# Kernel tuning notes

Hardware: AMD Instinct MI355X
Metric: run time of the kernel (lower is better)

The kernel has to match this reference:

```python
import jax, jax.numpy as jnp
import numpy as np

N = 16                      # input_dim (state dimension)
EPS = 1e-6
TRIL_R, TRIL_C = np.tril_indices(N)   # 136 lower-triangular slots


def setup_inputs() -> dict:
    key = jax.random.key(0)
    ks = jax.random.split(key, 7)
    B = 131072
    def xavier(k, fan_in, fan_out):
        lim = float(np.sqrt(6.0 / (fan_in + fan_out)))
        return jax.random.uniform(k, (fan_in, fan_out), jnp.float32, -lim, lim)
    return {
        "points": jax.random.normal(ks[0], (B, N), jnp.float32),
        "W0": xavier(ks[1], N, 512),
        "b0": jax.random.normal(ks[2], (512,), jnp.float32) * 0.01,
        "W1": xavier(ks[3], 512, 512),
        "b1": jax.random.normal(ks[4], (512,), jnp.float32) * 0.01,
        "W2": xavier(ks[5], 512, 136),
        "b2": jax.random.normal(ks[6], (136,), jnp.float32) * 0.01,
    }


def reference(points, W0, b0, W1, b1, W2, b2):
    # MLP: tanh, tanh, identity
    h = jnp.tanh(points @ W0 + b0)
    h = jnp.tanh(h @ W1 + b1)
    net = h @ W2 + b2                         # [B, 136] tril entries
    B = points.shape[0]
    # Batched scatter into lower-triangular matrices M: [B, N, N]
    M = jnp.zeros((B, N, N), points.dtype).at[:, TRIL_R, TRIL_C].set(net)
    # x^T (M M^T) x == ||M^T x||^2
    y = jnp.einsum('bij,bi->bj', M, points)   # (M^T x)_j = sum_i M_ij x_i
    vals = jnp.sum(y * y, axis=-1) + EPS * jnp.sum(points * points, axis=-1)
    return vals.reshape(-1, 1)
```

## Files before the change

kernel.cpp:

```cpp
#include <hip/hip_runtime.h>

typedef __bf16 bf16x4 __attribute__((ext_vector_type(4)));
typedef __bf16 bf16x8 __attribute__((ext_vector_type(8)));
typedef float f32x16 __attribute__((ext_vector_type(16)));

#define W0F_OFF 0
#define W1F_OFF 8192
#define W2F_OFF (8192 + 262144)
#define PREP_TOTAL (8192 + 262144 + 81920)

__global__ void prep_weights(const float* __restrict__ W0,
                             const float* __restrict__ W1,
                             const float* __restrict__ W2,
                             __bf16* __restrict__ ws) {
    int t = blockIdx.x * 256 + threadIdx.x;
    if (t < 8192) {
        int j = t & 7, lane = (t >> 3) & 63, nt = t >> 9;
        int n = nt * 32 + (lane & 31);
        int k = (lane >> 5) * 8 + j;
        ws[W0F_OFF + t] = (__bf16)W0[k * 512 + n];
    } else if (t < 8192 + 262144) {
        int u = t - 8192;
        int j = u & 7, lane = (u >> 3) & 63;
        int x = u >> 9;
        int kk = x & 31, nt = x >> 5;
        int n = nt * 32 + (lane & 31);
        int k = kk * 16 + (lane >> 5) * 8 + j;
        ws[W1F_OFF + u] = (__bf16)W1[k * 512 + n];
    } else if (t < PREP_TOTAL) {
        int v = t - (8192 + 262144);
        int j = v & 7, lane = (v >> 3) & 63;
        int x = v >> 9;
        int kk = x & 31, nt = x >> 5;
        int n = nt * 32 + (lane & 31);
        int k = kk * 16 + (lane >> 5) * 8 + j;
        ws[W2F_OFF + v] = (n < 136) ? (__bf16)W2[k * 136 + n] : (__bf16)0.0f;
    }
}

__device__ __forceinline__ float fast_tanh(float x) {
#if __has_builtin(__builtin_amdgcn_exp2f)
    float e = __builtin_amdgcn_exp2f(x * 2.885390081777926f);
#else
    float e = exp2f(x * 2.885390081777926f);
#endif
    return 1.0f - 2.0f * __builtin_amdgcn_rcpf(e + 1.0f);
}

#define HSTR 520
#define NSTR 140

__global__ __launch_bounds__(256, 2)
void fused_mlp_quad(const float* __restrict__ points,
                    const float* __restrict__ b0,
                    const float* __restrict__ b1,
                    const float* __restrict__ b2,
                    const __bf16* __restrict__ ws,
                    float* __restrict__ out) {
    __shared__ __align__(16) unsigned char lds_raw[33280];
    __bf16* h  = (__bf16*)lds_raw;
    float* net = (float*)lds_raw;

    const __bf16* w0f = ws + W0F_OFF;
    const __bf16* w1f = ws + W1F_OFF;
    const __bf16* w2f = ws + W2F_OFF;

    const int tid = threadIdx.x;
    const int w   = tid >> 6;
    const int l   = tid & 63;
    const int ln  = l & 31;
    const int hi  = l >> 5;
    const int row0 = blockIdx.x * 32;

    const int lofs = l * 8;

    {
        const float* src = points + (row0 + ln) * 16 + hi * 8;
        float4 p0 = ((const float4*)src)[0];
        float4 p1 = ((const float4*)src)[1];
        bf16x8 bx;
        bx[0] = (__bf16)p0.x; bx[1] = (__bf16)p0.y; bx[2] = (__bf16)p0.z; bx[3] = (__bf16)p0.w;
        bx[4] = (__bf16)p1.x; bx[5] = (__bf16)p1.y; bx[6] = (__bf16)p1.z; bx[7] = (__bf16)p1.w;
#pragma unroll
        for (int t = 0; t < 4; ++t) {
            const int ntg = w * 4 + t;
            bf16x8 wf = *(const bf16x8*)(w0f + ntg * 512 + lofs);
            f32x16 acc = {};
            acc = __builtin_amdgcn_mfma_f32_32x32x16_bf16(wf, bx, acc, 0, 0, 0);
#pragma unroll
            for (int rg = 0; rg < 4; ++rg) {
                const int n0 = ntg * 32 + 8 * rg + 4 * hi;
                float4 bias = *(const float4*)(b0 + n0);
                bf16x4 v;
                v[0] = (__bf16)fast_tanh(acc[4 * rg + 0] + bias.x);
                v[1] = (__bf16)fast_tanh(acc[4 * rg + 1] + bias.y);
                v[2] = (__bf16)fast_tanh(acc[4 * rg + 2] + bias.z);
                v[3] = (__bf16)fast_tanh(acc[4 * rg + 3] + bias.w);
                *(bf16x4*)(h + ln * HSTR + n0) = v;
            }
        }
    }
    __syncthreads();

    f32x16 acc1[4] = {};
    {
        const __bf16* arow = h + ln * HSTR + hi * 8;
        const __bf16* w1b0 = w1f + (w * 4 + 0) * 16384 + lofs;
        const __bf16* w1b1 = w1f + (w * 4 + 1) * 16384 + lofs;
        const __bf16* w1b2 = w1f + (w * 4 + 2) * 16384 + lofs;
        const __bf16* w1b3 = w1f + (w * 4 + 3) * 16384 + lofs;
        for (int ks = 0; ks < 16; ++ks) {
            bf16x8 aa[2], bb[2][4];
#pragma unroll
            for (int u = 0; u < 2; ++u) {
                const int kk = ks * 2 + u;
                const int vo = kk * 512;
                aa[u] = *(const bf16x8*)(arow + kk * 16);
                bb[u][0] = *(const bf16x8*)(w1b0 + vo);
                bb[u][1] = *(const bf16x8*)(w1b1 + vo);
                bb[u][2] = *(const bf16x8*)(w1b2 + vo);
                bb[u][3] = *(const bf16x8*)(w1b3 + vo);
            }
#pragma unroll
            for (int u = 0; u < 2; ++u) {
                acc1[0] = __builtin_amdgcn_mfma_f32_32x32x16_bf16(bb[u][0], aa[u], acc1[0], 0, 0, 0);
                acc1[1] = __builtin_amdgcn_mfma_f32_32x32x16_bf16(bb[u][1], aa[u], acc1[1], 0, 0, 0);
                acc1[2] = __builtin_amdgcn_mfma_f32_32x32x16_bf16(bb[u][2], aa[u], acc1[2], 0, 0, 0);
                acc1[3] = __builtin_amdgcn_mfma_f32_32x32x16_bf16(bb[u][3], aa[u], acc1[3], 0, 0, 0);
            }
        }
    }
    __syncthreads();
#pragma unroll
    for (int t = 0; t < 4; ++t) {
#pragma unroll
        for (int rg = 0; rg < 4; ++rg) {
            const int n0 = (w * 4 + t) * 32 + 8 * rg + 4 * hi;
            float4 bias = *(const float4*)(b1 + n0);
            bf16x4 v;
            v[0] = (__bf16)fast_tanh(acc1[t][4 * rg + 0] + bias.x);
            v[1] = (__bf16)fast_tanh(acc1[t][4 * rg + 1] + bias.y);
            v[2] = (__bf16)fast_tanh(acc1[t][4 * rg + 2] + bias.z);
            v[3] = (__bf16)fast_tanh(acc1[t][4 * rg + 3] + bias.w);
            *(bf16x4*)(h + ln * HSTR + n0) = v;
        }
    }
    __syncthreads();

    f32x16 acc2a = {}, acc2b = {};
    {
        const __bf16* arow = h + ln * HSTR + hi * 8;
        const bool two = (w == 0);
        const __bf16* w2bA = w2f + w * 16384 + lofs;
        const __bf16* w2bB = w2f + 4 * 16384 + lofs;
        for (int ks = 0; ks < 16; ++ks) {
            bf16x8 aa[2], bA[2], bB[2];
#pragma unroll
            for (int u = 0; u < 2; ++u) {
                const int kk = ks * 2 + u;
                const int vo = kk * 512;
                aa[u] = *(const bf16x8*)(arow + kk * 16);
                bA[u] = *(const bf16x8*)(w2bA + vo);
                if (two) bB[u] = *(const bf16x8*)(w2bB + vo);
            }
#pragma unroll
            for (int u = 0; u < 2; ++u) {
                acc2a = __builtin_amdgcn_mfma_f32_32x32x16_bf16(bA[u], aa[u], acc2a, 0, 0, 0);
                if (two)
                    acc2b = __builtin_amdgcn_mfma_f32_32x32x16_bf16(bB[u], aa[u], acc2b, 0, 0, 0);
            }
        }
    }
    __syncthreads();
    {
#pragma unroll
        for (int rg = 0; rg < 4; ++rg) {
            const int n0 = w * 32 + 8 * rg + 4 * hi;
            float4 bias = *(const float4*)(b2 + n0);
            float4 v;
            v.x = acc2a[4 * rg + 0] + bias.x;
            v.y = acc2a[4 * rg + 1] + bias.y;
            v.z = acc2a[4 * rg + 2] + bias.z;
            v.w = acc2a[4 * rg + 3] + bias.w;
            *(float4*)(net + ln * NSTR + n0) = v;
        }
        if (w == 0) {
            const int n0 = 128 + 4 * hi;
            float4 bias = *(const float4*)(b2 + n0);
            float4 v;
            v.x = acc2b[0] + bias.x;
            v.y = acc2b[1] + bias.y;
            v.z = acc2b[2] + bias.z;
            v.w = acc2b[3] + bias.w;
            *(float4*)(net + ln * NSTR + n0) = v;
        }
    }
    __syncthreads();

    {
        const int r  = tid >> 3;
        const int jg = tid & 7;
        const float* xp = points + (row0 + r) * 16;
        float xv[16];
#pragma unroll
        for (int i = 0; i < 4; ++i) {
            float4 v = ((const float4*)xp)[i];
            xv[i * 4 + 0] = v.x; xv[i * 4 + 1] = v.y;
            xv[i * 4 + 2] = v.z; xv[i * 4 + 3] = v.w;
        }
        float sumsq = 0.f;
#pragma unroll
        for (int i = 0; i < 16; ++i) sumsq += xv[i] * xv[i];
        float p = 0.f;
#pragma unroll
        for (int jj = 0; jj < 2; ++jj) {
            const int j = jg + jj * 8;
            float y = 0.f;
#pragma unroll
            for (int i = 0; i < 16; ++i) {
                float mv = net[r * NSTR + ((i * (i + 1)) >> 1) + j];
                y += (i >= j) ? mv * xv[i] : 0.f;
            }
            p += y * y;
        }
        p += __shfl_xor(p, 1);
        p += __shfl_xor(p, 2);
        p += __shfl_xor(p, 4);
        if (jg == 0) out[row0 + r] = p + 1e-6f * sumsq;
    }
}

extern "C" void kernel_launch(void* const* d_in, const int* in_sizes, int n_in,
                              void* d_out, int out_size, void* d_ws, size_t ws_size,
                              hipStream_t stream) {
    const float* points = (const float*)d_in[0];
    const float* W0 = (const float*)d_in[1];
    const float* b0 = (const float*)d_in[2];
    const float* W1 = (const float*)d_in[3];
    const float* b1 = (const float*)d_in[4];
    const float* W2 = (const float*)d_in[5];
    const float* b2 = (const float*)d_in[6];
    __bf16* ws = (__bf16*)d_ws;
    float* out = (float*)d_out;

    prep_weights<<<(PREP_TOTAL + 255) / 256, 256, 0, stream>>>(W0, W1, W2, ws);

    const int B = in_sizes[0] / 16;
    fused_mlp_quad<<<B / 32, 256, 0, stream>>>(points, b0, b1, b2, ws, out);
}
```

Measured before the change: 222.3 us.

## Process 64 rows per block to reuse weight fragments across two batch tiles

Result: slower. 400.2 us (+80.0%).

```diff
diff --git a/kernel.cpp b/kernel.cpp
--- a/kernel.cpp
+++ b/kernel.cpp
@@ -57,7 +57,7 @@
                     const float* __restrict__ b2,
                     const __bf16* __restrict__ ws,
                     float* __restrict__ out) {
-    __shared__ __align__(16) unsigned char lds_raw[33280];
+    __shared__ __align__(16) unsigned char lds_raw[66560];
     __bf16* h  = (__bf16*)lds_raw;
     float* net = (float*)lds_raw;
 
@@ -70,52 +70,62 @@
     const int l   = tid & 63;
     const int ln  = l & 31;
     const int hi  = l >> 5;
-    const int row0 = blockIdx.x * 32;
+    const int row0 = blockIdx.x * 64;
 
     const int lofs = l * 8;
 
     {
-        const float* src = points + (row0 + ln) * 16 + hi * 8;
-        float4 p0 = ((const float4*)src)[0];
-        float4 p1 = ((const float4*)src)[1];
-        bf16x8 bx;
-        bx[0] = (__bf16)p0.x; bx[1] = (__bf16)p0.y; bx[2] = (__bf16)p0.z; bx[3] = (__bf16)p0.w;
-        bx[4] = (__bf16)p1.x; bx[5] = (__bf16)p1.y; bx[6] = (__bf16)p1.z; bx[7] = (__bf16)p1.w;
+        bf16x8 bx[2];
+#pragma unroll
+        for (int bt = 0; bt < 2; ++bt) {
+            const float* src = points + (row0 + bt * 32 + ln) * 16 + hi * 8;
+            float4 p0 = ((const float4*)src)[0];
+            float4 p1 = ((const float4*)src)[1];
+            bf16x8 v;
+            v[0] = (__bf16)p0.x; v[1] = (__bf16)p0.y; v[2] = (__bf16)p0.z; v[3] = (__bf16)p0.w;
+            v[4] = (__bf16)p1.x; v[5] = (__bf16)p1.y; v[6] = (__bf16)p1.z; v[7] = (__bf16)p1.w;
+            bx[bt] = v;
+        }
 #pragma unroll
         for (int t = 0; t < 4; ++t) {
             const int ntg = w * 4 + t;
             bf16x8 wf = *(const bf16x8*)(w0f + ntg * 512 + lofs);
-            f32x16 acc = {};
-            acc = __builtin_amdgcn_mfma_f32_32x32x16_bf16(wf, bx, acc, 0, 0, 0);
-#pragma unroll
-            for (int rg = 0; rg < 4; ++rg) {
-                const int n0 = ntg * 32 + 8 * rg + 4 * hi;
-                float4 bias = *(const float4*)(b0 + n0);
-                bf16x4 v;
-                v[0] = (__bf16)fast_tanh(acc[4 * rg + 0] + bias.x);
-                v[1] = (__bf16)fast_tanh(acc[4 * rg + 1] + bias.y);
-                v[2] = (__bf16)fast_tanh(acc[4 * rg + 2] + bias.z);
-                v[3] = (__bf16)fast_tanh(acc[4 * rg + 3] + bias.w);
-                *(bf16x4*)(h + ln * HSTR + n0) = v;
-            }
-        }
-    }
-    __syncthreads();
-
-    f32x16 acc1[4] = {};
-    {
-        const __bf16* arow = h + ln * HSTR + hi * 8;
+#pragma unroll
+            for (int bt = 0; bt < 2; ++bt) {
+                f32x16 acc = {};
+                acc = __builtin_amdgcn_mfma_f32_32x32x16_bf16(wf, bx[bt], acc, 0, 0, 0);
+#pragma unroll
+                for (int rg = 0; rg < 4; ++rg) {
+                    const int n0 = ntg * 32 + 8 * rg + 4 * hi;
+                    float4 bias = *(const float4*)(b0 + n0);
+                    bf16x4 v;
+                    v[0] = (__bf16)fast_tanh(acc[4 * rg + 0] + bias.x);
+                    v[1] = (__bf16)fast_tanh(acc[4 * rg + 1] + bias.y);
+                    v[2] = (__bf16)fast_tanh(acc[4 * rg + 2] + bias.z);
+                    v[3] = (__bf16)fast_tanh(acc[4 * rg + 3] + bias.w);
+                    *(bf16x4*)(h + (bt * 32 + ln) * HSTR + n0) = v;
+                }
+            }
+        }
+    }
+    __syncthreads();
+
+    f32x16 acc1[2][4] = {};
+    {
+        const __bf16* arow0 = h + ln * HSTR + hi * 8;
+        const __bf16* arow1 = h + (32 + ln) * HSTR + hi * 8;
         const __bf16* w1b0 = w1f + (w * 4 + 0) * 16384 + lofs;
         const __bf16* w1b1 = w1f + (w * 4 + 1) * 16384 + lofs;
         const __bf16* w1b2 = w1f + (w * 4 + 2) * 16384 + lofs;
         const __bf16* w1b3 = w1f + (w * 4 + 3) * 16384 + lofs;
         for (int ks = 0; ks < 16; ++ks) {
-            bf16x8 aa[2], bb[2][4];
+            bf16x8 aa[2][2], bb[2][4];
 #pragma unroll
             for (int u = 0; u < 2; ++u) {
                 const int kk = ks * 2 + u;
                 const int vo = kk * 512;
-                aa[u] = *(const bf16x8*)(arow + kk * 16);
+                aa[u][0] = *(const bf16x8*)(arow0 + kk * 16);
+                aa[u][1] = *(const bf16x8*)(arow1 + kk * 16);
                 bb[u][0] = *(const bf16x8*)(w1b0 + vo);
                 bb[u][1] = *(const bf16x8*)(w1b1 + vo);
                 bb[u][2] = *(const bf16x8*)(w1b2 + vo);
@@ -123,10 +133,11 @@
             }
 #pragma unroll
             for (int u = 0; u < 2; ++u) {
-                acc1[0] = __builtin_amdgcn_mfma_f32_32x32x16_bf16(bb[u][0], aa[u], acc1[0], 0, 0, 0);
-                acc1[1] = __builtin_amdgcn_mfma_f32_32x32x16_bf16(bb[u][1], aa[u], acc1[1], 0, 0, 0);
-                acc1[2] = __builtin_amdgcn_mfma_f32_32x32x16_bf16(bb[u][2], aa[u], acc1[2], 0, 0, 0);
-                acc1[3] = __builtin_amdgcn_mfma_f32_32x32x16_bf16(bb[u][3], aa[u], acc1[3], 0, 0, 0);
+#pragma unroll
+                for (int t = 0; t < 4; ++t) {
+                    acc1[0][t] = __builtin_amdgcn_mfma_f32_32x32x16_bf16(bb[u][t], aa[u][0], acc1[0][t], 0, 0, 0);
+                    acc1[1][t] = __builtin_amdgcn_mfma_f32_32x32x16_bf16(bb[u][t], aa[u][1], acc1[1][t], 0, 0, 0);
+                }
             }
         }
     }
@@ -134,71 +145,81 @@
 #pragma unroll
     for (int t = 0; t < 4; ++t) {
 #pragma unroll
-        for (int rg = 0; rg < 4; ++rg) {
-            const int n0 = (w * 4 + t) * 32 + 8 * rg + 4 * hi;
-            float4 bias = *(const float4*)(b1 + n0);
-            bf16x4 v;
-            v[0] = (__bf16)fast_tanh(acc1[t][4 * rg + 0] + bias.x);
-            v[1] = (__bf16)fast_tanh(acc1[t][4 * rg + 1] + bias.y);
-            v[2] = (__bf16)fast_tanh(acc1[t][4 * rg + 2] + bias.z);
-            v[3] = (__bf16)fast_tanh(acc1[t][4 * rg + 3] + bias.w);
-            *(bf16x4*)(h + ln * HSTR + n0) = v;
-        }
-    }
-    __syncthreads();
-
-    f32x16 acc2a = {}, acc2b = {};
-    {
-        const __bf16* arow = h + ln * HSTR + hi * 8;
-        const bool two = (w == 0);
+        for (int bt = 0; bt < 2; ++bt) {
+#pragma unroll
+            for (int rg = 0; rg < 4; ++rg) {
+                const int n0 = (w * 4 + t) * 32 + 8 * rg + 4 * hi;
+                float4 bias = *(const float4*)(b1 + n0);
+                bf16x4 v;
+                v[0] = (__bf16)fast_tanh(acc1[bt][t][4 * rg + 0] + bias.x);
+                v[1] = (__bf16)fast_tanh(acc1[bt][t][4 * rg + 1] + bias.y);
+                v[2] = (__bf16)fast_tanh(acc1[bt][t][4 * rg + 2] + bias.z);
+                v[3] = (__bf16)fast_tanh(acc1[bt][t][4 * rg + 3] + bias.w);
+                *(bf16x4*)(h + (bt * 32 + ln) * HSTR + n0) = v;
+            }
+        }
+    }
+    __syncthreads();
+
+    f32x16 acc2[3] = {};
+    const bool three = (w < 2);
+    {
+        const __bf16* arow0 = h + ln * HSTR + hi * 8;
+        const __bf16* arow1 = h + (32 + ln) * HSTR + hi * 8;
         const __bf16* w2bA = w2f + w * 16384 + lofs;
         const __bf16* w2bB = w2f + 4 * 16384 + lofs;
         for (int ks = 0; ks < 16; ++ks) {
-            bf16x8 aa[2], bA[2], bB[2];
+            bf16x8 aa[2][2], wA[2], wB[2];
 #pragma unroll
             for (int u = 0; u < 2; ++u) {
                 const int kk = ks * 2 + u;
                 const int vo = kk * 512;
-                aa[u] = *(const bf16x8*)(arow + kk * 16);
-                bA[u] = *(const bf16x8*)(w2bA + vo);
-                if (two) bB[u] = *(const bf16x8*)(w2bB + vo);
-            }
-#pragma unroll
-            for (int u = 0; u < 2; ++u) {
-                acc2a = __builtin_amdgcn_mfma_f32_32x32x16_bf16(bA[u], aa[u], acc2a, 0, 0, 0);
-                if (two)
-                    acc2b = __builtin_amdgcn_mfma_f32_32x32x16_bf16(bB[u], aa[u], acc2b, 0, 0, 0);
-            }
-        }
-    }
-    __syncthreads();
-    {
-#pragma unroll
-        for (int rg = 0; rg < 4; ++rg) {
-            const int n0 = w * 32 + 8 * rg + 4 * hi;
-            float4 bias = *(const float4*)(b2 + n0);
-            float4 v;
-            v.x = acc2a[4 * rg + 0] + bias.x;
-            v.y = acc2a[4 * rg + 1] + bias.y;
-            v.z = acc2a[4 * rg + 2] + bias.z;
-            v.w = acc2a[4 * rg + 3] + bias.w;
-            *(float4*)(net + ln * NSTR + n0) = v;
-        }
-        if (w == 0) {
+                aa[u][0] = *(const bf16x8*)(arow0 + kk * 16);
+                aa[u][1] = *(const bf16x8*)(arow1 + kk * 16);
+                wA[u] = *(const bf16x8*)(w2bA + vo);
+                if (three) wB[u] = *(const bf16x8*)(w2bB + vo);
+            }
+#pragma unroll
+            for (int u = 0; u < 2; ++u) {
+                acc2[0] = __builtin_amdgcn_mfma_f32_32x32x16_bf16(wA[u], aa[u][0], acc2[0], 0, 0, 0);
+                acc2[1] = __builtin_amdgcn_mfma_f32_32x32x16_bf16(wA[u], aa[u][1], acc2[1], 0, 0, 0);
+                if (three)
+                    acc2[2] = __builtin_amdgcn_mfma_f32_32x32x16_bf16(wB[u], aa[u][w], acc2[2], 0, 0, 0);
+            }
+        }
+    }
+    __syncthreads();
+    {
+#pragma unroll
+        for (int bt = 0; bt < 2; ++bt) {
+#pragma unroll
+            for (int rg = 0; rg < 4; ++rg) {
+                const int n0 = w * 32 + 8 * rg + 4 * hi;
+                float4 bias = *(const float4*)(b2 + n0);
+                float4 v;
+                v.x = acc2[bt][4 * rg + 0] + bias.x;
+                v.y = acc2[bt][4 * rg + 1] + bias.y;
+                v.z = acc2[bt][4 * rg + 2] + bias.z;
+                v.w = acc2[bt][4 * rg + 3] + bias.w;
+                *(float4*)(net + (bt * 32 + ln) * NSTR + n0) = v;
+            }
+        }
+        if (three) {
             const int n0 = 128 + 4 * hi;
             float4 bias = *(const float4*)(b2 + n0);
             float4 v;
-            v.x = acc2b[0] + bias.x;
-            v.y = acc2b[1] + bias.y;
-            v.z = acc2b[2] + bias.z;
-            v.w = acc2b[3] + bias.w;
-            *(float4*)(net + ln * NSTR + n0) = v;
-        }
-    }
-    __syncthreads();
-
-    {
-        const int r  = tid >> 3;
+            v.x = acc2[2][0] + bias.x;
+            v.y = acc2[2][1] + bias.y;
+            v.z = acc2[2][2] + bias.z;
+            v.w = acc2[2][3] + bias.w;
+            *(float4*)(net + (w * 32 + ln) * NSTR + n0) = v;
+        }
+    }
+    __syncthreads();
+
+#pragma unroll
+    for (int half = 0; half < 2; ++half) {
+        const int r  = half * 32 + (tid >> 3);
         const int jg = tid & 7;
         const float* xp = points + (row0 + r) * 16;
         float xv[16];
@@ -246,5 +267,5 @@
     prep_weights<<<(PREP_TOTAL + 255) / 256, 256, 0, stream>>>(W0, W1, W2, ws);
 
     const int B = in_sizes[0] / 16;
-    fused_mlp_quad<<<B / 32, 256, 0, stream>>>(points, b0, b1, b2, ws, out);
-}
+    fused_mlp_quad<<<B / 64, 256, 0, stream>>>(points, b0, b1, b2, ws, out);
+}
```
